# Performance work log

Measured on AMD Instinct MI355X. Metric: run time of the kernel, lower is better.

Reference implementation:

```python
import jax, jax.numpy as jnp
import numpy as np

DIM = 768
N_HEADS = 12
HEAD_DIM = DIM // N_HEADS
SCALE = HEAD_DIM ** -0.5


def setup_inputs() -> dict:
    key = jax.random.key(0)
    kx, kqkv, kpw, kpb = jax.random.split(key, 4)
    B, N = 16, 1024
    x = jax.random.normal(kx, (B, N, DIM), dtype=jnp.float32)
    # nn.Linear weights stored [out, in]; torch computes x @ W.T + b
    w_qkv = jax.random.normal(kqkv, (3 * DIM, DIM), dtype=jnp.float32) * (DIM ** -0.5)
    w_proj = jax.random.normal(kpw, (DIM, DIM), dtype=jnp.float32) * (DIM ** -0.5)
    b_proj = jax.random.normal(kpb, (DIM,), dtype=jnp.float32) * 0.01
    return {"x": x, "w_qkv": w_qkv, "w_proj": w_proj, "b_proj": b_proj}


def reference(x, w_qkv, w_proj, b_proj):
    B, N, C = x.shape
    # qkv: [B, N, 3C] -> [3, B, H, N, Dh]
    qkv = (x @ w_qkv.T).reshape(B, N, 3, N_HEADS, HEAD_DIM)
    qkv = jnp.transpose(qkv, (2, 0, 3, 1, 4))
    q, k, v = qkv[0], qkv[1], qkv[2]
    # scores: [B, H, N, N]
    scores = jnp.einsum("bhnd,bhmd->bhnm", q, k) * SCALE
    attn = jax.nn.softmax(scores, axis=-1)
    out = jnp.einsum("bhnm,bhmd->bhnd", attn, v)
    out = jnp.transpose(out, (0, 2, 1, 3)).reshape(B, N, C)
    return out @ w_proj.T + b_proj
```

## Files before the change

kernel.cpp:

```cpp
#include <hip/hip_runtime.h>
#include <stdint.h>


typedef unsigned short u16;
typedef __attribute__((ext_vector_type(8))) short s16x8;
typedef __attribute__((ext_vector_type(4))) float f32x4;
typedef __attribute__((ext_vector_type(4))) unsigned short u16x4;

#define SEQ 1024
#define NHEAD 12
#define HD 64

__device__ __forceinline__ u16 f2bf(float f) {
  union { float f; uint32_t u; } v; v.f = f;
  uint32_t u = v.u;
  return (u16)((u + 0x7FFFu + ((u >> 16) & 1u)) >> 16);
}

__device__ __forceinline__ float exp2_fast(float x) {
  return __builtin_amdgcn_exp2f(x);
}

__device__ __forceinline__ uint32_t pk_bf16(float a, float b) {
#if __has_builtin(__builtin_amdgcn_cvt_pk_bf16_f32)
  typedef __attribute__((ext_vector_type(2))) __bf16 bf2;
  union { bf2 v; uint32_t u; } c;
  c.v = __builtin_amdgcn_cvt_pk_bf16_f32(a, b);
  return c.u;
#else
  union { float f; uint32_t u; } ua, ub; ua.f = a; ub.f = b;
  const uint32_t ra = ua.u + 0x8000u, rb = ub.u + 0x8000u;
  return __builtin_amdgcn_perm(ra, rb, 0x03020706u);
#endif
}

__device__ __forceinline__ void gld_lds16(const void* g, void* l) {
  __builtin_amdgcn_global_load_lds((const __attribute__((address_space(1))) void*)g,
                                   (__attribute__((address_space(3))) void*)l, 16, 0, 0);
}

__global__ void cvt_bf16_3(const float* __restrict__ in0, u16* __restrict__ out0, int n0,
                           const float* __restrict__ in1, u16* __restrict__ out1, int n1,
                           const float* __restrict__ in2, u16* __restrict__ out2, int n2) {
  int i = blockIdx.x * blockDim.x + threadIdx.x;
  const float* in; u16* out;
  if (i < n0)            { in = in0; out = out0; }
  else if (i < n0 + n1)  { in = in1; out = out1; i -= n0; }
  else if (i < n0 + n1 + n2) { in = in2; out = out2; i -= n0 + n1; }
  else return;
  float4 f = ((const float4*)in)[i];
  u16x4 o;
  o.x = f2bf(f.x); o.y = f2bf(f.y); o.z = f2bf(f.z); o.w = f2bf(f.w);
  ((u16x4*)out)[i] = o;
}

template <int EPI>
__global__ __launch_bounds__(256, 3)
void gemm_bt(const u16* __restrict__ A, const u16* __restrict__ B,
             u16* __restrict__ q, u16* __restrict__ k, u16* __restrict__ v,
             float* __restrict__ out, const float* __restrict__ bias) {
  __shared__ u16 As[128 * 64];
  __shared__ u16 Bs[128 * 64];
  const int tid = threadIdx.x;
  const int wv = tid >> 6, lane = tid & 63;
  const int quad = lane >> 4, l16 = lane & 15;
  const int m0 = blockIdx.x * 128, n0 = blockIdx.y * 128;
  const int wm = (wv & 1) * 64, wn = (wv >> 1) * 64;

  f32x4 acc[4][4];
#pragma unroll
  for (int i = 0; i < 4; i++)
#pragma unroll
    for (int j = 0; j < 4; j++) { acc[i][j].x = 0.f; acc[i][j].y = 0.f; acc[i][j].z = 0.f; acc[i][j].w = 0.f; }

  const int srow = (lane >> 3);
  const int scp = lane & 7;

  for (int kt = 0; kt < 768; kt += 64) {
    __syncthreads();
#pragma unroll
    for (int i = 0; i < 4; i++) {
      const int t = wv * 4 + i;
      const int row = t * 8 + srow;
      const int c = scp ^ (row & 7);
      gld_lds16(A + (size_t)(m0 + row) * 768 + kt + c * 8, &As[t * 512]);
      gld_lds16(B + (size_t)(n0 + row) * 768 + kt + c * 8, &Bs[t * 512]);
    }
    __syncthreads();
#pragma unroll
    for (int ks = 0; ks < 2; ks++) {
      s16x8 af[4], bf[4];
#pragma unroll
      for (int mi = 0; mi < 4; mi++) {
        const int ra = wm + mi * 16 + l16;
        const int ca = ((ks * 4 + quad) ^ (ra & 7)) * 8;
        af[mi] = *(const s16x8*)&As[ra * 64 + ca];
        const int rb = wn + mi * 16 + l16;
        const int cb = ((ks * 4 + quad) ^ (rb & 7)) * 8;
        bf[mi] = *(const s16x8*)&Bs[rb * 64 + cb];
      }
#pragma unroll
      for (int mi = 0; mi < 4; mi++)
#pragma unroll
        for (int ni = 0; ni < 4; ni++)
          acc[mi][ni] = __builtin_amdgcn_mfma_f32_16x16x32_bf16(af[mi], bf[ni], acc[mi][ni], 0, 0, 0);
    }
  }

  if (EPI == 0) {
#pragma unroll
    for (int ni = 0; ni < 4; ni++) {
      const int n = n0 + wn + ni * 16 + l16;
      const int which = n / 768;
      const int rc = n % 768;
      const int head = rc >> 6, d = rc & 63;
      if (which == 2) {
#pragma unroll
        for (int mi = 0; mi < 4; mi++) {
          const int mb = m0 + wm + mi * 16 + quad * 4;
          const int b = mb >> 10, rrb = mb & 1023;
          const int vcol = (rrb & ~31) | (((rrb >> 2) & 3) << 3) | (((rrb >> 4) & 1) << 2);
          u16x4 pk4;
          pk4.x = f2bf(acc[mi][ni][0]); pk4.y = f2bf(acc[mi][ni][1]);
          pk4.z = f2bf(acc[mi][ni][2]); pk4.w = f2bf(acc[mi][ni][3]);
          *(u16x4*)&v[((size_t)(b * NHEAD + head) * HD + d) * SEQ + vcol] = pk4;
        }
      } else {
#pragma unroll
        for (int mi = 0; mi < 4; mi++) {
#pragma unroll
          for (int r = 0; r < 4; r++) {
            const int m = m0 + wm + mi * 16 + quad * 4 + r;
            const int b = m >> 10, rr = m & 1023;
            const float val = acc[mi][ni][r];
            if (which == 0)
              q[((size_t)(b * NHEAD + head) * SEQ + rr) * HD + d] = f2bf(val * 0.18033688011112042f);
            else
              k[((size_t)(b * NHEAD + head) * SEQ + rr) * HD + d] = f2bf(val);
          }
        }
      }
    }
  } else {
#pragma unroll
    for (int mi = 0; mi < 4; mi++)
#pragma unroll
      for (int ni = 0; ni < 4; ni++)
#pragma unroll
        for (int r = 0; r < 4; r++) {
          const int m = m0 + wm + mi * 16 + quad * 4 + r;
          const int n = n0 + wn + ni * 16 + l16;
          out[(size_t)m * 768 + n] = acc[mi][ni][r] + bias[n];
        }
  }
}

__global__ __launch_bounds__(256, 3)
void flash_attn(const u16* __restrict__ Q, const u16* __restrict__ K,
                const u16* __restrict__ VT, u16* __restrict__ O) {
  __shared__ u16 Ks[2][64 * 64];
  __shared__ u16 Vs[2][64 * 64];

  const int tid = threadIdx.x;
  const int wv = tid >> 6, lane = tid & 63;
  const int quad = lane >> 4, l16 = lane & 15;
  const int bh = blockIdx.x;
  const int q0 = blockIdx.y * 128 + wv * 32;
  const size_t base = (size_t)bh * SEQ * HD;
  const size_t vbase = (size_t)bh * HD * SEQ;

  const int sr0 = tid >> 3;
  const int sc0 = (tid & 7) ^ (sr0 & 7);
  const int sr1 = 32 + sr0;
  const int sc1 = (tid & 7) ^ (sr1 & 7);

  s16x8 qf[2][2];
#pragma unroll
  for (int g = 0; g < 2; g++)
#pragma unroll
    for (int ks = 0; ks < 2; ks++)
      qf[g][ks] = *(const s16x8*)(Q + base + (size_t)(q0 + g * 16 + l16) * HD + ks * 32 + quad * 8);

  const s16x8 ones = {0x3F80, 0x3F80, 0x3F80, 0x3F80, 0x3F80, 0x3F80, 0x3F80, 0x3F80};

  f32x4 acc[2][4], acc_l[2];
#pragma unroll
  for (int g = 0; g < 2; g++) {
    acc_l[g].x = 0.f; acc_l[g].y = 0.f; acc_l[g].z = 0.f; acc_l[g].w = 0.f;
#pragma unroll
    for (int t = 0; t < 4; t++) { acc[g][t].x = 0.f; acc[g][t].y = 0.f; acc[g][t].z = 0.f; acc[g][t].w = 0.f; }
  }

  const int swz = l16 & 7;

  gld_lds16(K + base + (size_t)sr0 * HD + sc0 * 8, &Ks[0][wv * 512]);
  gld_lds16(VT + vbase + (size_t)sr0 * SEQ + sc0 * 8, &Vs[0][wv * 512]);
  gld_lds16(K + base + (size_t)sr1 * HD + sc1 * 8, &Ks[0][2048 + wv * 512]);
  gld_lds16(VT + vbase + (size_t)sr1 * SEQ + sc1 * 8, &Vs[0][2048 + wv * 512]);

  for (int it = 0; it < 16; it++) {
    __syncthreads();
    if (it + 1 < 16) {
      const int n1 = (it + 1) * 64;
      const int nb = (it + 1) & 1;
      gld_lds16(K + base + (size_t)(n1 + sr0) * HD + sc0 * 8, &Ks[nb][wv * 512]);
      gld_lds16(VT + vbase + (size_t)sr0 * SEQ + n1 + sc0 * 8, &Vs[nb][wv * 512]);
      gld_lds16(K + base + (size_t)(n1 + sr1) * HD + sc1 * 8, &Ks[nb][2048 + wv * 512]);
      gld_lds16(VT + vbase + (size_t)sr1 * SEQ + n1 + sc1 * 8, &Vs[nb][2048 + wv * 512]);
    }
    const u16* __restrict__ ks = Ks[it & 1];
    const u16* __restrict__ vs = Vs[it & 1];

    f32x4 s0[4], s1[4];
    __builtin_amdgcn_s_setprio(1);
#pragma unroll
    for (int t = 0; t < 4; t++) {
      s0[t].x = 0.f; s0[t].y = 0.f; s0[t].z = 0.f; s0[t].w = 0.f;
      s1[t].x = 0.f; s1[t].y = 0.f; s1[t].z = 0.f; s1[t].w = 0.f;
      const u16* kr = &ks[(t * 16 + l16) * 64];
      const s16x8 kf0 = *(const s16x8*)&kr[(quad ^ swz) * 8];
      const s16x8 kf1 = *(const s16x8*)&kr[((4 + quad) ^ swz) * 8];
      s0[t] = __builtin_amdgcn_mfma_f32_16x16x32_bf16(kf0, qf[0][0], s0[t], 0, 0, 0);
      s0[t] = __builtin_amdgcn_mfma_f32_16x16x32_bf16(kf1, qf[0][1], s0[t], 0, 0, 0);
      s1[t] = __builtin_amdgcn_mfma_f32_16x16x32_bf16(kf0, qf[1][0], s1[t], 0, 0, 0);
      s1[t] = __builtin_amdgcn_mfma_f32_16x16x32_bf16(kf1, qf[1][1], s1[t], 0, 0, 0);
    }
    __builtin_amdgcn_s_setprio(0);

#pragma unroll
    for (int t = 0; t < 4; t++)
#pragma unroll
      for (int r = 0; r < 4; r++) {
        s0[t][r] = exp2_fast(s0[t][r]);
        s1[t][r] = exp2_fast(s1[t][r]);
      }

    __builtin_amdgcn_s_setprio(1);
#pragma unroll
    for (int ks2 = 0; ks2 < 2; ks2++) {
      union { uint32_t w[4]; s16x8 v; } pa0, pa1;
      pa0.w[0] = pk_bf16(s0[2 * ks2][0], s0[2 * ks2][1]);
      pa0.w[1] = pk_bf16(s0[2 * ks2][2], s0[2 * ks2][3]);
      pa0.w[2] = pk_bf16(s0[2 * ks2 + 1][0], s0[2 * ks2 + 1][1]);
      pa0.w[3] = pk_bf16(s0[2 * ks2 + 1][2], s0[2 * ks2 + 1][3]);
      pa1.w[0] = pk_bf16(s1[2 * ks2][0], s1[2 * ks2][1]);
      pa1.w[1] = pk_bf16(s1[2 * ks2][2], s1[2 * ks2][3]);
      pa1.w[2] = pk_bf16(s1[2 * ks2 + 1][0], s1[2 * ks2 + 1][1]);
      pa1.w[3] = pk_bf16(s1[2 * ks2 + 1][2], s1[2 * ks2 + 1][3]);
      acc_l[0] = __builtin_amdgcn_mfma_f32_16x16x32_bf16(pa0.v, ones, acc_l[0], 0, 0, 0);
      acc_l[1] = __builtin_amdgcn_mfma_f32_16x16x32_bf16(pa1.v, ones, acc_l[1], 0, 0, 0);
      const int cp = ((ks2 * 4 + quad) ^ swz) * 8;
#pragma unroll
      for (int t2 = 0; t2 < 4; t2++) {
        const s16x8 vf = *(const s16x8*)&vs[(t2 * 16 + l16) * 64 + cp];
        acc[0][t2] = __builtin_amdgcn_mfma_f32_16x16x32_bf16(pa0.v, vf, acc[0][t2], 0, 0, 0);
        acc[1][t2] = __builtin_amdgcn_mfma_f32_16x16x32_bf16(pa1.v, vf, acc[1][t2], 0, 0, 0);
      }
    }
    __builtin_amdgcn_s_setprio(0);
  }

  const int b = bh / NHEAD, h = bh % NHEAD;
#pragma unroll
  for (int g = 0; g < 2; g++) {
#pragma unroll
    for (int r = 0; r < 4; r++) {
      const float li = 1.0f / acc_l[g][r];
      const int qrow = q0 + g * 16 + quad * 4 + r;
      u16* op = O + (size_t)(b * SEQ + qrow) * 768 + h * HD;
#pragma unroll
      for (int t2 = 0; t2 < 4; t2++)
        op[t2 * 16 + l16] = f2bf(acc[g][t2][r] * li);
    }
  }
}

extern "C" void kernel_launch(void* const* d_in, const int* in_sizes, int n_in,
                              void* d_out, int out_size, void* d_ws, size_t ws_size,
                              hipStream_t stream) {
  (void)in_sizes; (void)n_in; (void)out_size; (void)ws_size;
  const float* x      = (const float*)d_in[0];
  const float* w_qkv  = (const float*)d_in[1];
  const float* w_proj = (const float*)d_in[2];
  const float* b_proj = (const float*)d_in[3];

  const size_t SZ_X   = (size_t)16384 * 768;
  const size_t SZ_WQ  = (size_t)2304 * 768;
  const size_t SZ_WP  = (size_t)768 * 768;
  const size_t SZ_HED = (size_t)16 * NHEAD * SEQ * HD;

  u16* xb   = (u16*)d_ws;
  u16* wqb  = xb + SZ_X;
  u16* wpb  = wqb + SZ_WQ;
  u16* qb   = wpb + SZ_WP;
  u16* kb   = qb + SZ_HED;
  u16* vtb  = kb + SZ_HED;
  u16* attn = vtb + SZ_HED;

  const int n0 = (int)(SZ_X / 4), n1 = (int)(SZ_WQ / 4), n2 = (int)(SZ_WP / 4);
  const int nblk = (n0 + n1 + n2 + 255) / 256;
  cvt_bf16_3<<<nblk, 256, 0, stream>>>(x, xb, n0, w_qkv, wqb, n1, w_proj, wpb, n2);

  gemm_bt<0><<<dim3(128, 18), 256, 0, stream>>>(xb, wqb, qb, kb, vtb, nullptr, nullptr);
  flash_attn<<<dim3(192, 8), 256, 0, stream>>>(qb, kb, vtb, attn);
  gemm_bt<1><<<dim3(128, 6), 256, 0, stream>>>(attn, wpb, nullptr, nullptr, nullptr,
                                               (float*)d_out, b_proj);
}
```

Before: 261.7 us.

## Double query rows per warp and replace ones-MFMA row sums with VALU sums

```diff
diff --git a/kernel.cpp b/kernel.cpp
--- a/kernel.cpp
+++ b/kernel.cpp
@@ -32,6 +32,12 @@
   const uint32_t ra = ua.u + 0x8000u, rb = ub.u + 0x8000u;
   return __builtin_amdgcn_perm(ra, rb, 0x03020706u);
 #endif
+}
+
+__device__ __forceinline__ s16x8 mk8(uint32_t a, uint32_t b, uint32_t c, uint32_t d) {
+  union { uint32_t w[4]; s16x8 v; } u;
+  u.w[0] = a; u.w[1] = b; u.w[2] = c; u.w[3] = d;
+  return u.v;
 }
 
 __device__ __forceinline__ void gld_lds16(const void* g, void* l) {
@@ -165,7 +171,7 @@
   const int wv = tid >> 6, lane = tid & 63;
   const int quad = lane >> 4, l16 = lane & 15;
   const int bh = blockIdx.x;
-  const int q0 = blockIdx.y * 128 + wv * 32;
+  const int q0 = blockIdx.y * 256 + wv * 64;
   const size_t base = (size_t)bh * SEQ * HD;
   const size_t vbase = (size_t)bh * HD * SEQ;
 
@@ -174,22 +180,21 @@
   const int sr1 = 32 + sr0;
   const int sc1 = (tid & 7) ^ (sr1 & 7);
 
-  s16x8 qf[2][2];
-#pragma unroll
-  for (int g = 0; g < 2; g++)
+  s16x8 qf[4][2];
+#pragma unroll
+  for (int g = 0; g < 4; g++)
 #pragma unroll
     for (int ks = 0; ks < 2; ks++)
       qf[g][ks] = *(const s16x8*)(Q + base + (size_t)(q0 + g * 16 + l16) * HD + ks * 32 + quad * 8);
 
-  const s16x8 ones = {0x3F80, 0x3F80, 0x3F80, 0x3F80, 0x3F80, 0x3F80, 0x3F80, 0x3F80};
-
-  f32x4 acc[2][4], acc_l[2];
-#pragma unroll
-  for (int g = 0; g < 2; g++) {
-    acc_l[g].x = 0.f; acc_l[g].y = 0.f; acc_l[g].z = 0.f; acc_l[g].w = 0.f;
+  f32x4 acc[4][4];
+  float lp[4] = {0.f, 0.f, 0.f, 0.f};
+#pragma unroll
+  for (int g = 0; g < 4; g++)
 #pragma unroll
     for (int t = 0; t < 4; t++) { acc[g][t].x = 0.f; acc[g][t].y = 0.f; acc[g][t].z = 0.f; acc[g][t].w = 0.f; }
-  }
+
+  uint32_t paw[4][2][4];
 
   const int swz = l16 & 7;
 
@@ -211,50 +216,38 @@
     const u16* __restrict__ ks = Ks[it & 1];
     const u16* __restrict__ vs = Vs[it & 1];
 
-    f32x4 s0[4], s1[4];
     __builtin_amdgcn_s_setprio(1);
 #pragma unroll
     for (int t = 0; t < 4; t++) {
-      s0[t].x = 0.f; s0[t].y = 0.f; s0[t].z = 0.f; s0[t].w = 0.f;
-      s1[t].x = 0.f; s1[t].y = 0.f; s1[t].z = 0.f; s1[t].w = 0.f;
       const u16* kr = &ks[(t * 16 + l16) * 64];
       const s16x8 kf0 = *(const s16x8*)&kr[(quad ^ swz) * 8];
       const s16x8 kf1 = *(const s16x8*)&kr[((4 + quad) ^ swz) * 8];
-      s0[t] = __builtin_amdgcn_mfma_f32_16x16x32_bf16(kf0, qf[0][0], s0[t], 0, 0, 0);
-      s0[t] = __builtin_amdgcn_mfma_f32_16x16x32_bf16(kf1, qf[0][1], s0[t], 0, 0, 0);
-      s1[t] = __builtin_amdgcn_mfma_f32_16x16x32_bf16(kf0, qf[1][0], s1[t], 0, 0, 0);
-      s1[t] = __builtin_amdgcn_mfma_f32_16x16x32_bf16(kf1, qf[1][1], s1[t], 0, 0, 0);
+#pragma unroll
+      for (int g = 0; g < 4; g++) {
+        f32x4 s = {0.f, 0.f, 0.f, 0.f};
+        s = __builtin_amdgcn_mfma_f32_16x16x32_bf16(kf0, qf[g][0], s, 0, 0, 0);
+        s = __builtin_amdgcn_mfma_f32_16x16x32_bf16(kf1, qf[g][1], s, 0, 0, 0);
+        const float e0 = exp2_fast(s.x), e1 = exp2_fast(s.y);
+        const float e2 = exp2_fast(s.z), e3 = exp2_fast(s.w);
+        paw[g][t >> 1][(t & 1) * 2]     = pk_bf16(e0, e1);
+        paw[g][t >> 1][(t & 1) * 2 + 1] = pk_bf16(e2, e3);
+        lp[g] += (e0 + e1) + (e2 + e3);
+      }
     }
     __builtin_amdgcn_s_setprio(0);
 
-#pragma unroll
-    for (int t = 0; t < 4; t++)
-#pragma unroll
-      for (int r = 0; r < 4; r++) {
-        s0[t][r] = exp2_fast(s0[t][r]);
-        s1[t][r] = exp2_fast(s1[t][r]);
-      }
-
     __builtin_amdgcn_s_setprio(1);
 #pragma unroll
     for (int ks2 = 0; ks2 < 2; ks2++) {
-      union { uint32_t w[4]; s16x8 v; } pa0, pa1;
-      pa0.w[0] = pk_bf16(s0[2 * ks2][0], s0[2 * ks2][1]);
-      pa0.w[1] = pk_bf16(s0[2 * ks2][2], s0[2 * ks2][3]);
-      pa0.w[2] = pk_bf16(s0[2 * ks2 + 1][0], s0[2 * ks2 + 1][1]);
-      pa0.w[3] = pk_bf16(s0[2 * ks2 + 1][2], s0[2 * ks2 + 1][3]);
-      pa1.w[0] = pk_bf16(s1[2 * ks2][0], s1[2 * ks2][1]);
-      pa1.w[1] = pk_bf16(s1[2 * ks2][2], s1[2 * ks2][3]);
-      pa1.w[2] = pk_bf16(s1[2 * ks2 + 1][0], s1[2 * ks2 + 1][1]);
-      pa1.w[3] = pk_bf16(s1[2 * ks2 + 1][2], s1[2 * ks2 + 1][3]);
-      acc_l[0] = __builtin_amdgcn_mfma_f32_16x16x32_bf16(pa0.v, ones, acc_l[0], 0, 0, 0);
-      acc_l[1] = __builtin_amdgcn_mfma_f32_16x16x32_bf16(pa1.v, ones, acc_l[1], 0, 0, 0);
       const int cp = ((ks2 * 4 + quad) ^ swz) * 8;
 #pragma unroll
       for (int t2 = 0; t2 < 4; t2++) {
         const s16x8 vf = *(const s16x8*)&vs[(t2 * 16 + l16) * 64 + cp];
-        acc[0][t2] = __builtin_amdgcn_mfma_f32_16x16x32_bf16(pa0.v, vf, acc[0][t2], 0, 0, 0);
-        acc[1][t2] = __builtin_amdgcn_mfma_f32_16x16x32_bf16(pa1.v, vf, acc[1][t2], 0, 0, 0);
+#pragma unroll
+        for (int g = 0; g < 4; g++)
+          acc[g][t2] = __builtin_amdgcn_mfma_f32_16x16x32_bf16(
+              mk8(paw[g][ks2][0], paw[g][ks2][1], paw[g][ks2][2], paw[g][ks2][3]),
+              vf, acc[g][t2], 0, 0, 0);
       }
     }
     __builtin_amdgcn_s_setprio(0);
@@ -262,10 +255,13 @@
 
   const int b = bh / NHEAD, h = bh % NHEAD;
 #pragma unroll
-  for (int g = 0; g < 2; g++) {
+  for (int g = 0; g < 4; g++) {
+    float lf = lp[g];
+    lf += __shfl_xor(lf, 16);
+    lf += __shfl_xor(lf, 32);
 #pragma unroll
     for (int r = 0; r < 4; r++) {
-      const float li = 1.0f / acc_l[g][r];
+      const float li = 1.0f / __shfl(lf, quad * 4 + r);
       const int qrow = q0 + g * 16 + quad * 4 + r;
       u16* op = O + (size_t)(b * SEQ + qrow) * 768 + h * HD;
 #pragma unroll
@@ -302,7 +298,7 @@
   cvt_bf16_3<<<nblk, 256, 0, stream>>>(x, xb, n0, w_qkv, wqb, n1, w_proj, wpb, n2);
 
   gemm_bt<0><<<dim3(128, 18), 256, 0, stream>>>(xb, wqb, qb, kb, vtb, nullptr, nullptr);
-  flash_attn<<<dim3(192, 8), 256, 0, stream>>>(qb, kb, vtb, attn);
+  flash_attn<<<dim3(192, 4), 256, 0, stream>>>(qb, kb, vtb, attn);
   gemm_bt<1><<<dim3(128, 6), 256, 0, stream>>>(attn, wpb, nullptr, nullptr, nullptr,
                                                (float*)d_out, b_proj);
 }
```

After: 389.4 us. +48.8%, slower.
